# Optimization experiments

Hardware: AMD Instinct MI355X
Metric: run time of the kernel (lower is better)

## Reference

```python
import jax, jax.numpy as jnp
import numpy as np

N_HEAD = 16
N_EMBED = 2048


def setup_inputs() -> dict:
    key = jax.random.key(0)
    k1, k2, k3, k4, k5 = jax.random.split(key, 5)
    B, T, C = 4, 2048, N_EMBED
    scale = 1.0 / np.sqrt(C)
    return {
        "x": jax.random.normal(k1, (B, T, C), dtype=jnp.float32),
        "w_attn": jax.random.normal(k2, (C, 3 * C), dtype=jnp.float32) * scale,
        "b_attn": jnp.zeros((3 * C,), dtype=jnp.float32),
        "w_proj": jax.random.normal(k3, (C, C), dtype=jnp.float32) * scale,
        "b_proj": jnp.zeros((C,), dtype=jnp.float32),
    }


def reference(x, w_attn, b_attn, w_proj, b_proj):
    B, T, C = x.shape
    H = N_HEAD
    hd = C // H
    # fused QKV projection: [B,T,3C]
    qkv = jnp.einsum("btc,cd->btd", x, w_attn) + b_attn
    q, k, v = jnp.split(qkv, 3, axis=-1)
    # [B,H,T,hd]
    q = q.reshape(B, T, H, hd).transpose(0, 2, 1, 3)
    k = k.reshape(B, T, H, hd).transpose(0, 2, 1, 3)
    v = v.reshape(B, T, H, hd).transpose(0, 2, 1, 3)
    # scaled dot-product attention (no mask, no dropout at eval)
    scores = jnp.einsum("bhqd,bhkd->bhqk", q, k) / jnp.sqrt(jnp.asarray(hd, dtype=q.dtype))
    attn = jax.nn.softmax(scores, axis=-1)
    y = jnp.einsum("bhqk,bhkd->bhqd", attn, v)
    y = y.transpose(0, 2, 1, 3).reshape(B, T, C)
    return jnp.einsum("btc,cd->btd", y, w_proj) + b_proj
```

## Files before the change

### kernel.cpp

```cpp
#include <hip/hip_runtime.h>
#include <hip/hip_fp16.h>

typedef _Float16 f16;
typedef _Float16 half8 __attribute__((ext_vector_type(8)));
typedef float f32x4 __attribute__((ext_vector_type(4)));

#define NBAT 4
#define NT   2048
#define NC   2048
#define NHEAD 16
#define HD   128
#define NM   8192
#define N3C  6144
#define QK_LD 4096
#define ATT_SCALE 0.088388347648318447f

static __device__ __forceinline__ void gload16(const void* g, void* l) {
  __builtin_amdgcn_global_load_lds(
      (const __attribute__((address_space(1))) unsigned int*)g,
      (__attribute__((address_space(3))) unsigned int*)l, 16, 0, 0);
}


__global__ __launch_bounds__(256) void cvt_x_f16(const float* __restrict__ in,
                                                 f16* __restrict__ out) {
  size_t i = ((size_t)blockIdx.x * 256 + threadIdx.x) * 8;
  float4 a = *(const float4*)(in + i);
  float4 b = *(const float4*)(in + i + 4);
  half8 o;
  o[0] = (f16)a.x; o[1] = (f16)a.y; o[2] = (f16)a.z; o[3] = (f16)a.w;
  o[4] = (f16)b.x; o[5] = (f16)b.y; o[6] = (f16)b.z; o[7] = (f16)b.w;
  *(half8*)(out + i) = o;
}

__global__ __launch_bounds__(256) void cvt_tr_f16(const float* __restrict__ in,
                                                  f16* __restrict__ out,
                                                  int R, int CC) {
  __shared__ float tile[32][33];
  int cb = blockIdx.x * 32, rb = blockIdx.y * 32;
  int lx = threadIdx.x & 31, ly = threadIdx.x >> 5;
  for (int i = 0; i < 32; i += 8)
    tile[ly + i][lx] = in[(size_t)(rb + ly + i) * CC + cb + lx];
  __syncthreads();
  for (int i = 0; i < 32; i += 8)
    out[(size_t)(cb + ly + i) * R + rb + lx] = (f16)tile[lx][ly + i];
}

template <int OUTMODE>
__global__ __launch_bounds__(512, 2)
void gemm256(const f16* __restrict__ A, const f16* __restrict__ BT,
             const float* __restrict__ bias,
             f16* __restrict__ oqk, f16* __restrict__ ovT,
             float* __restrict__ of32, int N, int K, int nbn) {
  __shared__ f16 sA[4 * 8192];
  __shared__ f16 sB[4 * 8192];

  const int tid = threadIdx.x;
  const int wv = tid >> 6, lane = tid & 63;
  const int lr = lane & 15, lg = lane >> 4;
  const int wm = wv >> 2, wn = wv & 3;

  const int q8 = gridDim.x >> 3;
  const int sid = ((int)blockIdx.x & 7) * q8 + ((int)blockIdx.x >> 3);
  const int bm = sid / nbn, bn = sid % nbn;

  const int q0 = tid >> 3;
  const int cx = (tid & 7) ^ (q0 & 7);
  const f16* aSrc = A + (size_t)(bm * 256 + q0) * K + cx * 8;
  const f16* bSrc = BT + (size_t)(bn * 256 + q0) * K + cx * 8;
  const size_t rs64 = (size_t)64 * K, rs128 = (size_t)128 * K;

  const int NKT = K >> 6, NIT = NKT >> 1;
  f32x4 acc[8][4] = {};

  auto stgA = [&](int t, int h, int bu) {
    const f16* s = aSrc + (size_t)h * rs128 + t * 64;
    f16* d = sA + (bu * 2 + h) * 8192 + tid * 8;
    gload16(s, d);
    gload16(s + rs64, d + 4096);
  };
  auto stgB = [&](int t, int h, int bu) {
    const f16* s = bSrc + (size_t)h * rs128 + t * 64;
    f16* d = sB + (bu * 2 + h) * 8192 + tid * 8;
    gload16(s, d);
    gload16(s + rs64, d + 4096);
  };

  stgA(0, 0, 0); stgA(0, 1, 0);
  stgB(0, 0, 0); stgB(0, 1, 0);
  stgB(1, 0, 1); stgB(1, 1, 1);
  asm volatile("s_waitcnt vmcnt(4)" ::: "memory");
  __builtin_amdgcn_s_barrier();
  asm volatile("" ::: "memory");

  const int xcs[2] = {((0 * 4 + lg) ^ (lr & 7)) * 8, ((1 * 4 + lg) ^ (lr & 7)) * 8};

  for (int it = 0; it < NIT; ++it) {
    const int u = 2 * it, v = u + 1;
    const bool notlast = (it < NIT - 1);
    half8 bfrag[4][2];
#pragma unroll
    for (int p = 0; p < 8; ++p) {
      const int buf = (p < 4) ? 0 : 1;
      const f16* bA = sA + (buf * 2 + wm) * 8192;
      const f16* bB = sB + (buf * 2 + (wn >> 1)) * 8192;
      const int mf0 = (p & 3) * 2;
      if ((p & 3) == 0) {
#pragma unroll
        for (int nf = 0; nf < 4; ++nf)
#pragma unroll
          for (int ks = 0; ks < 2; ++ks)
            bfrag[nf][ks] = *(const half8*)(
                bB + ((wn & 1) * 64 + nf * 16 + lr) * 64 + xcs[ks]);
      }
      half8 afrag[2][2];
#pragma unroll
      for (int m2 = 0; m2 < 2; ++m2)
#pragma unroll
        for (int ks = 0; ks < 2; ++ks)
          afrag[m2][ks] = *(const half8*)(
              bA + ((mf0 + m2) * 16 + lr) * 64 + xcs[ks]);
      switch (p) {
        case 0: stgA(v, 0, 1); break;
        case 1: stgA(v, 1, 1); break;
        case 2: if (notlast) stgB(u + 2, 0, 0); break;
        case 3: if (notlast) stgB(u + 2, 1, 0); break;
        case 4: if (notlast) stgA(u + 2, 0, 0); break;
        case 5: if (notlast) stgA(u + 2, 1, 0); break;
        case 6: if (notlast) stgB(v + 2, 0, 1); break;
        case 7: if (notlast) stgB(v + 2, 1, 1); break;
      }
      if ((p & 3) == 3) {
        if (notlast) asm volatile("s_waitcnt vmcnt(4)" ::: "memory");
        else         asm volatile("s_waitcnt vmcnt(0)" ::: "memory");
      }
      asm volatile("" ::: "memory");
      __builtin_amdgcn_s_barrier();
      asm volatile("" ::: "memory");
      __builtin_amdgcn_s_setprio(1);
#pragma unroll
      for (int m2 = 0; m2 < 2; ++m2)
#pragma unroll
        for (int nf = 0; nf < 4; ++nf)
#pragma unroll
          for (int ks = 0; ks < 2; ++ks)
            acc[mf0 + m2][nf] = __builtin_amdgcn_mfma_f32_16x16x32_f16(
                afrag[m2][ks], bfrag[nf][ks], acc[mf0 + m2][nf], 0, 0, 0);
      __builtin_amdgcn_s_setprio(0);
      asm volatile("" ::: "memory");
      __builtin_amdgcn_s_barrier();
    }
  }

#pragma unroll
  for (int nf = 0; nf < 4; ++nf) {
    const int col = bn * 256 + wn * 64 + nf * 16 + lr;
    const float bv = bias[col];
#pragma unroll
    for (int mf = 0; mf < 8; ++mf) {
      const int row0 = bm * 256 + wm * 128 + mf * 16 + lg * 4;
      f32x4 v = acc[mf][nf];
      if (OUTMODE == 0) {
#pragma unroll
        for (int r = 0; r < 4; ++r)
          of32[(size_t)(row0 + r) * N + col] = v[r] + bv;
      } else {
        if (col < 4096) {
#pragma unroll
          for (int r = 0; r < 4; ++r)
            oqk[(size_t)(row0 + r) * QK_LD + col] = (f16)(v[r] + bv);
        } else {
          const int dfull = col - 4096;
          const int hh = dfull >> 7, dd = dfull & 127;
#pragma unroll
          for (int r = 0; r < 4; ++r) {
            const int row = row0 + r;
            const int bb = row >> 11, tt = row & 2047;
            ovT[((size_t)(bb * NHEAD + hh) * HD + dd) * NT + tt] = (f16)(v[r] + bv);
          }
        }
      }
    }
  }
}

__global__ __launch_bounds__(256, 2)
void attn_fwd(const f16* __restrict__ qk, const f16* __restrict__ vT,
              f16* __restrict__ y) {
  const int bid = blockIdx.x;
  const int sid = (bid & 7) * 128 + (bid >> 3);
  const int qt = sid & 15;
  const int bh = sid >> 4;
  const int b = bh >> 4, h = bh & 15;
  const int tid = threadIdx.x, w = tid >> 6, lane = tid & 63;
  const int lr = lane & 15, lg = lane >> 4;

  __shared__ f16 Ks[2][64 * 128];
  __shared__ f16 Vs[2][128 * 64];
  __shared__ f16 Ps[4][2][16 * 64];

  half8 qf[2][4];
  for (int s = 0; s < 2; ++s) {
    const f16* qp = qk + (size_t)(b * NT + qt * 128 + w * 32 + s * 16 + lr) * QK_LD +
                    h * HD + lg * 8;
    for (int dc = 0; dc < 4; ++dc) qf[s][dc] = *(const half8*)(qp + dc * 32);
  }

  f32x4 accy[2][8] = {};
  f32x4 lacc[2] = {};
  float mrow[2][4];
  for (int s = 0; s < 2; ++s)
    for (int r = 0; r < 4; ++r) mrow[s][r] = -1e30f;

  half8 onev;
  for (int j = 0; j < 8; ++j) onev[j] = (f16)1.0f;

  const char* kbase[4];
  const char* vbase[4];
  for (int j = 0; j < 4; ++j) {
    int idx = w * 4 + j;
    {
      int row = idx * 4 + lg;
      int swz = (lr * 16) ^ ((row & 7) << 4);
      kbase[j] = (const char*)qk +
                 ((size_t)(b * NT + row) * QK_LD + 2048 + h * HD) * 2 + swz;
    }
    {
      int d = idx * 8 + (lane >> 3);
      int cj = (lane & 7) ^ (d & 7);
      vbase[j] = (const char*)vT + ((size_t)(bh * HD + d) * NT + cj * 8) * 2;
    }
  }

  for (int j = 0; j < 4; ++j) {
    int idx = w * 4 + j;
    gload16(kbase[j], (void*)((char*)Ks[0] + idx * 1024));
    gload16(vbase[j], (void*)((char*)Vs[0] + idx * 1024));
  }

  int cur = 0;
  for (int kt = 0; kt < 32; ++kt) {
    if (kt + 1 < 32) {
      for (int j = 0; j < 4; ++j) {
        int idx = w * 4 + j;
        gload16(kbase[j] + (size_t)(kt + 1) * (64 * QK_LD * 2),
                (void*)((char*)Ks[cur ^ 1] + idx * 1024));
        gload16(vbase[j] + (size_t)(kt + 1) * 128,
                (void*)((char*)Vs[cur ^ 1] + idx * 1024));
      }
    }
    if (kt < 31) asm volatile("s_waitcnt vmcnt(8)" ::: "memory");
    else         asm volatile("s_waitcnt vmcnt(0)" ::: "memory");
    __builtin_amdgcn_s_barrier();
    asm volatile("" ::: "memory");

    f32x4 sa[2][4] = {};
    for (int nb = 0; nb < 4; ++nb) {
      int kvr = nb * 16 + lr;
      const char* kr = (const char*)Ks[cur] + kvr * 256;
      int s7 = (kvr & 7) << 4;
      for (int dc = 0; dc < 4; ++dc) {
        half8 kb = *(const half8*)(kr + ((dc * 64 + lg * 16) ^ s7));
        sa[0][nb] = __builtin_amdgcn_mfma_f32_16x16x32_f16(qf[0][dc], kb, sa[0][nb], 0, 0, 0);
        sa[1][nb] = __builtin_amdgcn_mfma_f32_16x16x32_f16(qf[1][dc], kb, sa[1][nb], 0, 0, 0);
      }
    }

    for (int s = 0; s < 2; ++s) {
      float sv[4][4];
      float pml[4] = {-1e30f, -1e30f, -1e30f, -1e30f};
      for (int nb = 0; nb < 4; ++nb)
        for (int r = 0; r < 4; ++r) {
          float x = sa[s][nb][r] * ATT_SCALE;
          sv[nb][r] = x;
          pml[r] = fmaxf(pml[r], x);
        }
      bool ok = true;
      for (int r = 0; r < 4; ++r) ok &= (pml[r] <= mrow[s][r] + 8.0f);
      if (!__all(ok)) {
        for (int r = 0; r < 4; ++r) {
          for (int off = 1; off < 16; off <<= 1)
            pml[r] = fmaxf(pml[r], __shfl_xor(pml[r], off));
          float mn = fmaxf(mrow[s][r], pml[r]);
          float al = __expf(mrow[s][r] - mn);
          mrow[s][r] = mn;
          lacc[s][r] *= al;
          for (int db = 0; db < 8; ++db) accy[s][db][r] *= al;
        }
      }
      for (int nb = 0; nb < 4; ++nb)
        for (int r = 0; r < 4; ++r) {
          float p = __expf(sv[nb][r] - mrow[s][r]);
          int prow = lg * 4 + r;
          int chunk = (nb * 2 + (lr >> 3)) ^ (prow & 7);
          Ps[w][s][prow * 64 + chunk * 8 + (lr & 7)] = (f16)p;
        }
    }

    half8 pa[2][2];
    for (int s = 0; s < 2; ++s)
      for (int kc = 0; kc < 2; ++kc) {
        int chunk = (kc * 4 + lg) ^ (lr & 7);
        pa[s][kc] = *(const half8*)(&Ps[w][s][lr * 64 + chunk * 8]);
      }
    for (int s = 0; s < 2; ++s)
      for (int kc = 0; kc < 2; ++kc)
        lacc[s] = __builtin_amdgcn_mfma_f32_16x16x32_f16(pa[s][kc], onev, lacc[s], 0, 0, 0);

    for (int db = 0; db < 8; ++db) {
      int d = db * 16 + lr;
      const char* vr = (const char*)Vs[cur] + d * 128;
      int d7 = d & 7;
      for (int kc = 0; kc < 2; ++kc) {
        half8 vb = *(const half8*)(vr + (((kc * 4 + lg) ^ d7) * 16));
        accy[0][db] = __builtin_amdgcn_mfma_f32_16x16x32_f16(pa[0][kc], vb, accy[0][db], 0, 0, 0);
        accy[1][db] = __builtin_amdgcn_mfma_f32_16x16x32_f16(pa[1][kc], vb, accy[1][db], 0, 0, 0);
      }
    }

    asm volatile("" ::: "memory");
    __builtin_amdgcn_s_barrier();
    cur ^= 1;
  }

  for (int s = 0; s < 2; ++s) {
    f32x4 inv;
    for (int r = 0; r < 4; ++r) inv[r] = 1.0f / lacc[s][r];
    f16* yp = y + (size_t)(b * NT + qt * 128 + w * 32 + s * 16 + lg * 4) * NC +
              h * HD + lr;
    for (int db = 0; db < 8; ++db)
      for (int r = 0; r < 4; ++r)
        yp[(size_t)r * NC + db * 16] = (f16)(accy[s][db][r] * inv[r]);
  }
}

extern "C" void kernel_launch(void* const* d_in, const int* in_sizes, int n_in,
                              void* d_out, int out_size, void* d_ws, size_t ws_size,
                              hipStream_t stream) {
  (void)in_sizes; (void)n_in; (void)out_size; (void)ws_size;
  const float* x      = (const float*)d_in[0];
  const float* w_attn = (const float*)d_in[1];
  const float* b_attn = (const float*)d_in[2];
  const float* w_proj = (const float*)d_in[3];
  const float* b_proj = (const float*)d_in[4];
  float* out = (float*)d_out;

  char* p = (char*)d_ws;
  f16* xh  = (f16*)p; p += (size_t)NM * NC * 2;
  f16* waT = (f16*)p; p += (size_t)N3C * NC * 2;
  f16* wpT = (f16*)p; p += (size_t)NC * NC * 2;
  f16* qkb = (f16*)p; p += (size_t)NM * QK_LD * 2;
  f16* vT  = (f16*)p; p += (size_t)NBAT * NHEAD * HD * NT * 2;
  f16* yh  = (f16*)p; p += (size_t)NM * NC * 2;

  cvt_x_f16<<<8192, 256, 0, stream>>>(x, xh);
  cvt_tr_f16<<<dim3(192, 64), 256, 0, stream>>>(w_attn, waT, NC, N3C);
  cvt_tr_f16<<<dim3(64, 64), 256, 0, stream>>>(w_proj, wpT, NC, NC);
  gemm256<1><<<768, 512, 0, stream>>>(xh, waT, b_attn, qkb, vT, nullptr,
                                      N3C, NC, 24);
  attn_fwd<<<1024, 256, 0, stream>>>(qkb, vT, yh);
  gemm256<0><<<256, 512, 0, stream>>>(yh, wpT, b_proj, nullptr, nullptr,
                                      out, NC, NC, 8);
}
```

Measured before the change: 483.7 us.

## Remap GEMM tiles per XCD, vectorize V-transpose stores, compute row sums via shuffles

Replaces the GEMM block-to-tile mapping with an explicit 2D grouping in which each XCD covers a contiguous 8-row by half-width block of output tiles, aiming at better L2 reuse of A and B panels. The transposed V output is written as packed 4-element f16 vectors instead of four scalar stores. In attention, the softmax row sum is now accumulated in fp32 from the exp values with a cross-lane shuffle reduction, replacing the extra MFMA against a ones vector. The shuffles add VALU and cross-lane work, and the sum now comes from unrounded fp32 values rather than the f16 P that feeds the PV product, which shifts numerics slightly. The new tile mapping assumes fixed grid dimensions (32 row tiles).

Measured after the change: 515.2 us. 1.07x slower.

```diff
diff --git a/kernel.cpp b/kernel.cpp
--- a/kernel.cpp
+++ b/kernel.cpp
@@ -3,6 +3,7 @@
 
 typedef _Float16 f16;
 typedef _Float16 half8 __attribute__((ext_vector_type(8)));
+typedef _Float16 half4v __attribute__((ext_vector_type(4)));
 typedef float f32x4 __attribute__((ext_vector_type(4)));
 
 #define NBAT 4
@@ -60,9 +61,10 @@
   const int lr = lane & 15, lg = lane >> 4;
   const int wm = wv >> 2, wn = wv & 3;
 
-  const int q8 = gridDim.x >> 3;
-  const int sid = ((int)blockIdx.x & 7) * q8 + ((int)blockIdx.x >> 3);
-  const int bm = sid / nbn, bn = sid % nbn;
+  const int bid = blockIdx.x;
+  const int xcd = bid & 7, li = bid >> 3;
+  const int bm = (xcd & 3) * 8 + (li & 7);
+  const int bn = (xcd >> 2) * (nbn >> 1) + (li >> 3);
 
   const int q0 = tid >> 3;
   const int cx = (tid & 7) ^ (q0 & 7);
@@ -172,12 +174,11 @@
         } else {
           const int dfull = col - 4096;
           const int hh = dfull >> 7, dd = dfull & 127;
-#pragma unroll
-          for (int r = 0; r < 4; ++r) {
-            const int row = row0 + r;
-            const int bb = row >> 11, tt = row & 2047;
-            ovT[((size_t)(bb * NHEAD + hh) * HD + dd) * NT + tt] = (f16)(v[r] + bv);
-          }
+          const int bb = row0 >> 11, tt0 = row0 & 2047;
+          half4v pk;
+#pragma unroll
+          for (int r = 0; r < 4; ++r) pk[r] = (f16)(v[r] + bv);
+          *(half4v*)(ovT + ((size_t)(bb * NHEAD + hh) * HD + dd) * NT + tt0) = pk;
         }
       }
     }
@@ -207,13 +208,10 @@
   }
 
   f32x4 accy[2][8] = {};
-  f32x4 lacc[2] = {};
+  float lsum[2][4] = {};
   float mrow[2][4];
   for (int s = 0; s < 2; ++s)
     for (int r = 0; r < 4; ++r) mrow[s][r] = -1e30f;
-
-  half8 onev;
-  for (int j = 0; j < 8; ++j) onev[j] = (f16)1.0f;
 
   const char* kbase[4];
   const char* vbase[4];
@@ -284,17 +282,23 @@
           float mn = fmaxf(mrow[s][r], pml[r]);
           float al = __expf(mrow[s][r] - mn);
           mrow[s][r] = mn;
-          lacc[s][r] *= al;
+          lsum[s][r] *= al;
           for (int db = 0; db < 8; ++db) accy[s][db][r] *= al;
         }
       }
+      float rs[4] = {0.f, 0.f, 0.f, 0.f};
       for (int nb = 0; nb < 4; ++nb)
         for (int r = 0; r < 4; ++r) {
           float p = __expf(sv[nb][r] - mrow[s][r]);
+          rs[r] += p;
           int prow = lg * 4 + r;
           int chunk = (nb * 2 + (lr >> 3)) ^ (prow & 7);
           Ps[w][s][prow * 64 + chunk * 8 + (lr & 7)] = (f16)p;
         }
+      for (int r = 0; r < 4; ++r) {
+        for (int off = 1; off < 16; off <<= 1) rs[r] += __shfl_xor(rs[r], off);
+        lsum[s][r] += rs[r];
+      }
     }
 
     half8 pa[2][2];
@@ -303,9 +307,6 @@
         int chunk = (kc * 4 + lg) ^ (lr & 7);
         pa[s][kc] = *(const half8*)(&Ps[w][s][lr * 64 + chunk * 8]);
       }
-    for (int s = 0; s < 2; ++s)
-      for (int kc = 0; kc < 2; ++kc)
-        lacc[s] = __builtin_amdgcn_mfma_f32_16x16x32_f16(pa[s][kc], onev, lacc[s], 0, 0, 0);
 
     for (int db = 0; db < 8; ++db) {
       int d = db * 16 + lr;
@@ -325,7 +326,7 @@
 
   for (int s = 0; s < 2; ++s) {
     f32x4 inv;
-    for (int r = 0; r < 4; ++r) inv[r] = 1.0f / lacc[s][r];
+    for (int r = 0; r < 4; ++r) inv[r] = 1.0f / lsum[s][r];
     f16* yp = y + (size_t)(b * NT + qt * 128 + w * 32 + s * 16 + lg * 4) * NC +
               h * HD + lr;
     for (int db = 0; db < 8; ++db)
```
